# Kernel tuning notes

Measured on AMD Instinct MI355X. Metric: run time of the kernel, lower is better.

## Reference

```python
import jax, jax.numpy as jnp
import numpy as np

N_ENTITIES = 100000
EMBED = 64
BATCH = 4096
TEMPERATURE = 0.2


def _infonce(v1, v2, temperature):
    # v1, v2: [B, d]
    B = v1.shape[0]
    sim11 = v1 @ v1.T  # [B,B]
    sim22 = v2 @ v2.T
    sim12 = v1 @ v2.T
    eye = jnp.eye(B, dtype=bool)
    neg_inf = jnp.float32(-jnp.inf)
    sim11 = jnp.where(eye, neg_inf, sim11)
    sim22 = jnp.where(eye, neg_inf, sim22)
    logits1 = jnp.concatenate([sim12, sim11], axis=-1)          # [B,2B]
    logits2 = jnp.concatenate([sim22, sim12.T], axis=-1)        # [B,2B]
    logits = jnp.concatenate([logits1, logits2], axis=0) / temperature  # [2B,2B]
    targets = jnp.arange(2 * B)
    logp = jax.nn.log_softmax(logits, axis=-1)
    return -jnp.mean(jnp.take_along_axis(logp, targets[:, None], axis=-1))


def setup_inputs() -> dict:
    key = jax.random.key(0)
    k1, k2, k3, k4, k5, k6 = jax.random.split(key, 6)
    return {
        "input_u_list": jax.random.randint(k1, (BATCH,), 0, N_ENTITIES),
        "input_i_list": jax.random.randint(k2, (BATCH,), 0, N_ENTITIES),
        "u_sub1_embeddings": jax.random.normal(k3, (N_ENTITIES, EMBED), dtype=jnp.float32),
        "i_sub1_embeddings": jax.random.normal(k4, (N_ENTITIES, EMBED), dtype=jnp.float32),
        "u_sub2_embeddings": jax.random.normal(k5, (N_ENTITIES, EMBED), dtype=jnp.float32),
        "i_sub2_embeddings": jax.random.normal(k6, (N_ENTITIES, EMBED), dtype=jnp.float32),
    }


def reference(input_u_list, input_i_list, u_sub1_embeddings, i_sub1_embeddings,
              u_sub2_embeddings, i_sub2_embeddings):
    # user branch: gather + L2-normalize
    u1 = u_sub1_embeddings[input_u_list]
    u2 = u_sub2_embeddings[input_u_list]
    u1 = u1 / jnp.linalg.norm(u1, axis=1, keepdims=True)
    u2 = u2 / jnp.linalg.norm(u2, axis=1, keepdims=True)
    user_cl_loss = _infonce(u1, u2, TEMPERATURE)
    # item branch: gather only (the original does NOT normalize items)
    i1 = i_sub1_embeddings[input_i_list]
    i2 = i_sub2_embeddings[input_i_list]
    item_cl_loss = _infonce(i1, i2, TEMPERATURE)
    return user_cl_loss + item_cl_loss
```

## Files before the change

kernel.cpp:

```cpp
#include <hip/hip_runtime.h>
#include <hip/hip_bf16.h>
#include <math.h>

#define B_SZ   4096
#define D      64
#define RPB    8192
#define NCHUNK 8
#define TPC    8
#define NPART  16
#define LN2    0.69314718055994531f
#define PRESCALE 2.6857914f
#define DEFER_THR 60.0f

typedef __attribute__((ext_vector_type(8))) short  bf16x8;
typedef __attribute__((ext_vector_type(4))) float  f32x4;

__device__ __forceinline__ float fexp2(float x) { return __builtin_amdgcn_exp2f(x); }

typedef const __attribute__((address_space(1))) unsigned int* gptr_t;
typedef __attribute__((address_space(3))) unsigned int* lptr_t;
__device__ __forceinline__ void stage16(const void* g, void* l) {
    __builtin_amdgcn_global_load_lds((gptr_t)g, (lptr_t)l, 16, 0, 0);
}


__global__ __launch_bounds__(256) void gather_kernel(
    const int* __restrict__ u_idx, const int* __restrict__ i_idx,
    const float* __restrict__ u1e, const float* __restrict__ i1e,
    const float* __restrict__ u2e, const float* __restrict__ i2e,
    __hip_bfloat16* __restrict__ Xbf, float* __restrict__ dots,
    float* __restrict__ out)
{
    const int tid  = threadIdx.x;
    if (blockIdx.x == 0 && tid == 0) *out = 0.f;
    const int wave = tid >> 6, lane = tid & 63;
    const int g      = blockIdx.x * 4 + wave;
    const int branch = g >> 12;
    const int i      = g & (B_SZ - 1);
    const int idx    = (branch == 0) ? u_idx[i] : i_idx[i];
    const float* s1  = (branch == 0) ? u1e : i1e;
    const float* s2  = (branch == 0) ? u2e : i2e;

    float v1 = s1[(size_t)idx * D + lane];
    float v2 = s2[(size_t)idx * D + lane];
    if (branch == 0) {
        float a = v1 * v1, b = v2 * v2;
        #pragma unroll
        for (int o = 32; o > 0; o >>= 1) {
            a += __shfl_xor(a, o, 64);
            b += __shfl_xor(b, o, 64);
        }
        v1 *= rsqrtf(a);
        v2 *= rsqrtf(b);
    }
    float p = v1 * v2;
    #pragma unroll
    for (int o = 32; o > 0; o >>= 1) p += __shfl_xor(p, o, 64);
    if (lane == 0) dots[g] = p;

    const size_t row1 = (size_t)branch * RPB + i;
    Xbf[row1 * D + lane]          = __float2bfloat16(v1 * PRESCALE);
    Xbf[(row1 + B_SZ) * D + lane] = __float2bfloat16(v2 * PRESCALE);
}

template<int IS_USER>
__device__ __forceinline__ void gram_body(
    const __hip_bfloat16* __restrict__ Xb, float2* __restrict__ P,
    const int bx, char* sm)
{
    const int tid   = threadIdx.x;
    const int chunk = blockIdx.y;
    const int r0    = bx * 128;
    const int wave = tid >> 6, lane = tid & 63;
    const int wm = wave >> 1, wn = wave & 1;
    const int quad = lane >> 4, tx = lane & 15;

    const int srow_b = wave * 32 + (lane >> 3);
    const int scb    = ((lane & 7) * 16) ^ ((lane >> 3) << 4);
    const char* Xbytes = (const char*)Xb;

    {
        const char* src = Xbytes + (size_t)(chunk * TPC) * 16384;
        #pragma unroll
        for (int k = 0; k < 4; ++k)
            stage16(src + (srow_b + k * 8) * 128 + scb,
                    sm + wave * 4096 + k * 1024);
    }

    bf16x8 afr[4][2];
    const __hip_bfloat16* Ap = Xb + (size_t)(r0 + wm * 64 + tx) * D + quad * 8;
    #pragma unroll
    for (int mt = 0; mt < 4; ++mt)
        #pragma unroll
        for (int ks = 0; ks < 2; ++ks)
            afr[mt][ks] = *(const bf16x8*)(Ap + mt * 16 * D + ks * 32);

    float m_run[16], s_run[16];
    #pragma unroll
    for (int r = 0; r < 16; ++r) { m_run[r] = 0.f; s_run[r] = 0.f; }

    const int lrq  = wm * 64 + quad * 4;
    const int lcol = wn * 64 + tx;

    const int rbase = (wn * 64 + tx) * 128;
    const int key   = (tx & 7) << 4;
    const int cb0   = (quad * 16) ^ key;
    const int cb1   = (64 + quad * 16) ^ key;

    __syncthreads();

    #pragma unroll 1
    for (int t = 0; t < TPC; ++t) {
        const int ct  = chunk * TPC + t;
        const int cur = (t & 1) << 14;

        if (t + 1 < TPC) {
            const char* src = Xbytes + (size_t)(ct + 1) * 16384;
            char* dst = sm + (((t + 1) & 1) << 14) + wave * 4096;
            #pragma unroll
            for (int k = 0; k < 4; ++k)
                stage16(src + (srow_b + k * 8) * 128 + scb, dst + k * 1024);
        }

        const bool diag = (ct == bx);
        const f32x4 z = {0.f, 0.f, 0.f, 0.f};

        #pragma unroll
        for (int nt = 0; nt < 4; ++nt) {
            const bf16x8 b0 = *(const bf16x8*)(sm + cur + rbase + nt * 2048 + cb0);
            const bf16x8 b1 = *(const bf16x8*)(sm + cur + rbase + nt * 2048 + cb1);
            f32x4 acc[4];
            #pragma unroll
            for (int mt = 0; mt < 4; ++mt)
                acc[mt] = __builtin_amdgcn_mfma_f32_16x16x32_bf16(afr[mt][0], b0, z, 0, 0, 0);
            #pragma unroll
            for (int mt = 0; mt < 4; ++mt)
                acc[mt] = __builtin_amdgcn_mfma_f32_16x16x32_bf16(afr[mt][1], b1, acc[mt], 0, 0, 0);

            #pragma unroll
            for (int mt = 0; mt < 4; ++mt) {
                #pragma unroll
                for (int rr = 0; rr < 4; ++rr) {
                    float y = acc[mt][rr];
                    if (diag && (lrq + mt * 16 + rr - lcol == nt * 16))
                        y = -INFINITY;
                    const int r = mt * 4 + rr;
                    if (IS_USER) {
                        s_run[r] += fexp2(y);
                    } else {
                        if (__builtin_expect(y > m_run[r] + DEFER_THR, 0)) {
                            s_run[r] *= fexp2(m_run[r] - y);
                            m_run[r] = y;
                        }
                        s_run[r] += fexp2(y - m_run[r]);
                    }
                }
            }
        }

        __syncthreads();
    }

    #pragma unroll
    for (int r = 0; r < 16; ++r) {
        float m = IS_USER ? 0.f : m_run[r];
        float s = s_run[r];
        #pragma unroll
        for (int o = 1; o < 16; o <<= 1) {
            if (IS_USER) {
                s += __shfl_xor(s, o, 64);
            } else {
                float om = __shfl_xor(m, o, 64);
                float os = __shfl_xor(s, o, 64);
                float M  = fmaxf(m, om);
                s = s * fexp2(m - M) + os * fexp2(om - M);
                m = M;
            }
        }
        if (tx == 0) {
            const int grow = r0 + wm * 64 + (r >> 2) * 16 + quad * 4 + (r & 3);
            P[(size_t)grow * NPART + chunk * 2 + wn] = make_float2(m, s);
        }
    }
}

__global__ __launch_bounds__(256, 2) void gram_lse_fused(
    const __hip_bfloat16* __restrict__ Xb0, float2* __restrict__ P0)
{
    __shared__ __align__(16) char sm[32768];
    const int branch = blockIdx.x & 1;
    const int bx     = blockIdx.x >> 1;
    const __hip_bfloat16* Xb = Xb0 + (size_t)branch * RPB * D;
    float2* P = P0 + (size_t)branch * RPB * NPART;
    if (branch == 0) gram_body<1>(Xb, P, bx, sm);
    else             gram_body<0>(Xb, P, bx, sm);
}

__global__ __launch_bounds__(256) void merge_kernel(
    const float2* __restrict__ P, const float* __restrict__ dots,
    float* __restrict__ out)
{
    __shared__ float red[4];
    const int tid  = threadIdx.x;
    const int wave = tid >> 6, lane = tid & 63;

    float vsum = 0.f;
    #pragma unroll
    for (int k = 0; k < 8; ++k) {
        const int vb  = blockIdx.x * 8 + k;
        const int gw  = vb * 4 + wave;
        const int row = gw * 4 + (lane >> 4);
        const int c   = lane & 15;

        float2 p = P[(size_t)row * NPART + c];
        float m = p.x, s = p.y;
        #pragma unroll
        for (int o = 1; o < 16; o <<= 1) {
            float om = __shfl_xor(m, o, 64);
            float os = __shfl_xor(s, o, 64);
            float M  = fmaxf(m, om);
            s = s * fexp2(m - M) + os * fexp2(om - M);
            m = M;
        }

        if ((lane & 15) == 0)
            vsum += LN2 * (m + log2f(s)) * (1.0f / (float)RPB);
        if (tid < 8)
            vsum -= dots[vb * 8 + tid] * (5.0f / (float)B_SZ);
    }

    float v = vsum;
    #pragma unroll
    for (int o = 32; o > 0; o >>= 1) v += __shfl_xor(v, o, 64);
    if (lane == 0) red[wave] = v;
    __syncthreads();
    if (tid == 0)
        atomicAdd(out, red[0] + red[1] + red[2] + red[3]);
}

extern "C" void kernel_launch(void* const* d_in, const int* in_sizes, int n_in,
                              void* d_out, int out_size, void* d_ws, size_t ws_size,
                              hipStream_t stream) {
    const int*   u_idx = (const int*)d_in[0];
    const int*   i_idx = (const int*)d_in[1];
    const float* u1e   = (const float*)d_in[2];
    const float* i1e   = (const float*)d_in[3];
    const float* u2e   = (const float*)d_in[4];
    const float* i2e   = (const float*)d_in[5];
    float* out = (float*)d_out;

    __hip_bfloat16* Xbf = (__hip_bfloat16*)d_ws;
    float*  dots = (float*)((char*)d_ws + 2 * RPB * D * 2);
    float2* P    = (float2*)((char*)dots + RPB * sizeof(float));

    gather_kernel<<<dim3(2048), dim3(256), 0, stream>>>(
        u_idx, i_idx, u1e, i1e, u2e, i2e, Xbf, dots, out);
    gram_lse_fused<<<dim3(128, NCHUNK), dim3(256), 0, stream>>>(Xbf, P);
    merge_kernel<<<dim3(128), dim3(256), 0, stream>>>(P, dots, out);
}
```

Measured before the change: 202.3 us.

## Split gram-LSE column work into more chunks and pair MFMA tiles for ILP

Doubles the number of column chunks per row block (fewer tiles per chunk, more partial LSE slots) and raises the launch-bounds occupancy hint from 2 to 3 blocks per CU, to expose more parallel blocks. Inside the tile loop, two column sub-tiles are processed together so their MFMA chains interleave, and the online max/sum update runs once per pair. The merge kernel is reworked to reduce 32 partials per row, and the running max now starts at -inf. The costs are more partial results to write and merge, and more register pressure from the paired accumulators.

```diff
diff --git a/kernel.cpp b/kernel.cpp
--- a/kernel.cpp
+++ b/kernel.cpp
@@ -5,9 +5,9 @@
 #define B_SZ   4096
 #define D      64
 #define RPB    8192
-#define NCHUNK 8
-#define TPC    8
-#define NPART  16
+#define NCHUNK 16
+#define TPC    4
+#define NPART  32
 #define LN2    0.69314718055994531f
 #define PRESCALE 2.6857914f
 #define DEFER_THR 60.0f
@@ -97,7 +97,7 @@
 
     float m_run[16], s_run[16];
     #pragma unroll
-    for (int r = 0; r < 16; ++r) { m_run[r] = 0.f; s_run[r] = 0.f; }
+    for (int r = 0; r < 16; ++r) { m_run[r] = -INFINITY; s_run[r] = 0.f; }
 
     const int lrq  = wm * 64 + quad * 4;
     const int lcol = wn * 64 + tx;
@@ -126,33 +126,47 @@
         const f32x4 z = {0.f, 0.f, 0.f, 0.f};
 
         #pragma unroll
-        for (int nt = 0; nt < 4; ++nt) {
-            const bf16x8 b0 = *(const bf16x8*)(sm + cur + rbase + nt * 2048 + cb0);
-            const bf16x8 b1 = *(const bf16x8*)(sm + cur + rbase + nt * 2048 + cb1);
-            f32x4 acc[4];
-            #pragma unroll
-            for (int mt = 0; mt < 4; ++mt)
-                acc[mt] = __builtin_amdgcn_mfma_f32_16x16x32_bf16(afr[mt][0], b0, z, 0, 0, 0);
-            #pragma unroll
-            for (int mt = 0; mt < 4; ++mt)
-                acc[mt] = __builtin_amdgcn_mfma_f32_16x16x32_bf16(afr[mt][1], b1, acc[mt], 0, 0, 0);
+        for (int h = 0; h < 2; ++h) {
+            const int ntA = 2 * h, ntB = 2 * h + 1;
+            const bf16x8 bA0 = *(const bf16x8*)(sm + cur + rbase + ntA * 2048 + cb0);
+            const bf16x8 bA1 = *(const bf16x8*)(sm + cur + rbase + ntA * 2048 + cb1);
+            const bf16x8 bB0 = *(const bf16x8*)(sm + cur + rbase + ntB * 2048 + cb0);
+            const bf16x8 bB1 = *(const bf16x8*)(sm + cur + rbase + ntB * 2048 + cb1);
+
+            f32x4 accA[4], accB[4];
+            #pragma unroll
+            for (int mt = 0; mt < 4; ++mt)
+                accA[mt] = __builtin_amdgcn_mfma_f32_16x16x32_bf16(afr[mt][0], bA0, z, 0, 0, 0);
+            #pragma unroll
+            for (int mt = 0; mt < 4; ++mt)
+                accB[mt] = __builtin_amdgcn_mfma_f32_16x16x32_bf16(afr[mt][0], bB0, z, 0, 0, 0);
+            #pragma unroll
+            for (int mt = 0; mt < 4; ++mt)
+                accA[mt] = __builtin_amdgcn_mfma_f32_16x16x32_bf16(afr[mt][1], bA1, accA[mt], 0, 0, 0);
+            #pragma unroll
+            for (int mt = 0; mt < 4; ++mt)
+                accB[mt] = __builtin_amdgcn_mfma_f32_16x16x32_bf16(afr[mt][1], bB1, accB[mt], 0, 0, 0);
 
             #pragma unroll
             for (int mt = 0; mt < 4; ++mt) {
                 #pragma unroll
                 for (int rr = 0; rr < 4; ++rr) {
-                    float y = acc[mt][rr];
-                    if (diag && (lrq + mt * 16 + rr - lcol == nt * 16))
-                        y = -INFINITY;
+                    float y0 = accA[mt][rr], y1 = accB[mt][rr];
+                    if (diag) {
+                        const int dr = lrq + mt * 16 + rr - lcol;
+                        if (dr == h * 32)      y0 = -INFINITY;
+                        if (dr == h * 32 + 16) y1 = -INFINITY;
+                    }
                     const int r = mt * 4 + rr;
                     if (IS_USER) {
-                        s_run[r] += fexp2(y);
+                        s_run[r] += fexp2(y0) + fexp2(y1);
                     } else {
-                        if (__builtin_expect(y > m_run[r] + DEFER_THR, 0)) {
-                            s_run[r] *= fexp2(m_run[r] - y);
-                            m_run[r] = y;
+                        float mx = fmaxf(y0, y1);
+                        if (__builtin_expect(mx > m_run[r] + DEFER_THR, 0)) {
+                            s_run[r] *= fexp2(m_run[r] - mx);
+                            m_run[r] = mx;
                         }
-                        s_run[r] += fexp2(y - m_run[r]);
+                        s_run[r] += fexp2(y0 - m_run[r]) + fexp2(y1 - m_run[r]);
                     }
                 }
             }
@@ -184,7 +198,7 @@
     }
 }
 
-__global__ __launch_bounds__(256, 2) void gram_lse_fused(
+__global__ __launch_bounds__(256, 3) void gram_lse_fused(
     const __hip_bfloat16* __restrict__ Xb0, float2* __restrict__ P0)
 {
     __shared__ __align__(16) char sm[32768];
@@ -206,16 +220,14 @@
 
     float vsum = 0.f;
     #pragma unroll
-    for (int k = 0; k < 8; ++k) {
-        const int vb  = blockIdx.x * 8 + k;
-        const int gw  = vb * 4 + wave;
-        const int row = gw * 4 + (lane >> 4);
-        const int c   = lane & 15;
+    for (int it = 0; it < 16; ++it) {
+        const int row = blockIdx.x * 128 + it * 8 + wave * 2 + (lane >> 5);
+        const int c   = lane & 31;
 
         float2 p = P[(size_t)row * NPART + c];
         float m = p.x, s = p.y;
         #pragma unroll
-        for (int o = 1; o < 16; o <<= 1) {
+        for (int o = 1; o < 32; o <<= 1) {
             float om = __shfl_xor(m, o, 64);
             float os = __shfl_xor(s, o, 64);
             float M  = fmaxf(m, om);
@@ -223,11 +235,12 @@
             m = M;
         }
 
-        if ((lane & 15) == 0)
+        if ((lane & 31) == 0)
             vsum += LN2 * (m + log2f(s)) * (1.0f / (float)RPB);
-        if (tid < 8)
-            vsum -= dots[vb * 8 + tid] * (5.0f / (float)B_SZ);
-    }
+    }
+
+    if (tid < 64)
+        vsum -= dots[blockIdx.x * 64 + tid] * (5.0f / (float)B_SZ);
 
     float v = vsum;
     #pragma unroll
```

Measured after the change: 185.2 us. -8.5%, faster.
